# Performance work log

Measured on AMD Instinct MI355X. Metric: run time of the kernel, lower is better.

The kernel has to match this reference:

```python
import jax, jax.numpy as jnp
import numpy as np

B, L, D, H, DFF = 4, 2048, 1024, 16, 4096
DH = D // H  # head dim = 64
EPS = 1e-5


def layernorm(x, g, b):
    mu = jnp.mean(x, axis=-1, keepdims=True)
    var = jnp.mean(jnp.square(x - mu), axis=-1, keepdims=True)
    return (x - mu) * jax.lax.rsqrt(var + EPS) * g + b


def setup_inputs() -> dict:
    key = jax.random.key(0)
    ks = jax.random.split(key, 16)
    s = 0.02
    return {
        "X": jax.random.normal(ks[0], (B, L, D), jnp.float32),
        "WQ": jax.random.normal(ks[1], (D, D), jnp.float32) * s,
        "bQ": jnp.zeros((D,), jnp.float32),
        "WK": jax.random.normal(ks[2], (D, D), jnp.float32) * s,
        "bK": jnp.zeros((D,), jnp.float32),
        "WV": jax.random.normal(ks[3], (D, D), jnp.float32) * s,
        "bV": jnp.zeros((D,), jnp.float32),
        "WO": jax.random.normal(ks[4], (D, D), jnp.float32) * s,
        "bO": jnp.zeros((D,), jnp.float32),
        "W1": jax.random.normal(ks[5], (D, DFF), jnp.float32) * s,
        "b1": jnp.zeros((DFF,), jnp.float32),
        "W2": jax.random.normal(ks[6], (DFF, D), jnp.float32) * s,
        "b2": jnp.zeros((D,), jnp.float32),
        "g1": jnp.ones((D,), jnp.float32),
        "be1": jnp.zeros((D,), jnp.float32),
        "g2": jnp.ones((D,), jnp.float32),
        "be2": jnp.zeros((D,), jnp.float32),
    }


def reference(X, WQ, bQ, WK, bK, WV, bV, WO, bO, W1, b1, W2, b2, g1, be1, g2, be2):
    # --- causal self-attention on LayerNorm1(X) ---
    Xn = layernorm(X, g1, be1)
    def heads(W, b):
        return (Xn @ W + b).reshape(B, L, H, DH).transpose(0, 2, 1, 3)  # [B,H,L,DH]
    Q, K, V = heads(WQ, bQ), heads(WK, bK), heads(WV, bV)
    scale = 1.0 / jnp.sqrt(jnp.float32(DH))
    scores = jnp.einsum('bhld,bhsd->bhls', Q, K) * scale  # [B,H,L,L]
    causal = jnp.tril(jnp.ones((L, L), dtype=bool))
    scores = jnp.where(causal, scores, -jnp.inf)
    attn = jax.nn.softmax(scores, axis=-1)
    AV = jnp.einsum('bhls,bhsd->bhld', attn, V)  # [B,H,L,DH]
    AV = AV.transpose(0, 2, 1, 3).reshape(B, L, H * DH)
    X = X + AV @ WO + bO
    # --- MLP on LayerNorm2(X) ---
    Xn2 = layernorm(X, g2, be2)
    out = X + jax.nn.relu(Xn2 @ W1 + b1) @ W2 + b2
    return out
```

## Files before the change

kernel.cpp:

```cpp
#include <hip/hip_runtime.h>
#include <hip/hip_bf16.h>
#include <stdint.h>

#define B_   4
#define L_   2048
#define D_   1024
#define H_   16
#define DH_  64
#define DFF_ 4096
#define EPS_ 1e-5f

typedef short s16x8 __attribute__((ext_vector_type(8)));
typedef short s16x4 __attribute__((ext_vector_type(4)));
typedef float f32x4 __attribute__((ext_vector_type(4)));

static __device__ __forceinline__ short f2bf(float f) {
    return __builtin_bit_cast(short, __float2bfloat16(f));
}

static __device__ __forceinline__ void gload_lds16(const void* g, void* l) {
    __builtin_amdgcn_global_load_lds(
        (const __attribute__((address_space(1))) uint32_t*)g,
        (__attribute__((address_space(3))) uint32_t*)l, 16, 0, 0);
}

__global__ __launch_bounds__(256) void transpose_kernel(
    const float* __restrict__ in, short* __restrict__ out, int R, int C)
{
    __shared__ float tile[32][33];
    const int bx = blockIdx.x * 32, by = blockIdx.y * 32;
    const int tx = threadIdx.x & 31, ty = threadIdx.x >> 5;
#pragma unroll
    for (int i = 0; i < 32; i += 8)
        tile[ty + i][tx] = in[(size_t)(by + ty + i) * C + bx + tx];
    __syncthreads();
#pragma unroll
    for (int i = 0; i < 32; i += 8)
        out[(size_t)(bx + ty + i) * R + by + tx] = f2bf(tile[tx][ty + i]);
}

__global__ __launch_bounds__(256) void concat3_kernel(
    const float* __restrict__ a, const float* __restrict__ b,
    const float* __restrict__ c, float* __restrict__ o)
{
    const int i = blockIdx.x * 256 + threadIdx.x;
    o[i] = (i < 1024) ? a[i] : (i < 2048 ? b[i - 1024] : c[i - 2048]);
}

__global__ __launch_bounds__(256) void vtrans_kernel(
    const short* __restrict__ V, short* __restrict__ Vt)
{
    __shared__ short t[64][72];
    const int l0 = blockIdx.x * 64;
    const int bh = blockIdx.y;
    const int b = bh >> 4, h = bh & 15;
    const int tid = threadIdx.x;
    const int rr = tid >> 3, cc = tid & 7;
#pragma unroll
    for (int i = 0; i < 2; ++i) {
        const int row = i * 32 + rr;
        *(s16x8*)&t[row][cc * 8] =
            *(const s16x8*)(V + (size_t)(b * L_ + l0 + row) * D_ + h * DH_ + cc * 8);
    }
    __syncthreads();
#pragma unroll
    for (int i = 0; i < 2; ++i) {
        const int d = i * 32 + rr;
        const int lp0 = cc * 8;
        s16x8 o;
#pragma unroll
        for (int j = 0; j < 8; ++j) o[j] = t[lp0 + j][d];
        *(s16x8*)(Vt + ((size_t)bh * DH_ + d) * L_ + l0 + lp0) = o;
    }
}

__global__ __launch_bounds__(256) void ln_kernel(
    const float* __restrict__ x, const float* __restrict__ g,
    const float* __restrict__ bta, short* __restrict__ out)
{
    __shared__ float sm[8];
    const int row = blockIdx.x;
    const int t = threadIdx.x;
    const float4 v = ((const float4*)(x + (size_t)row * D_))[t];
    float s1 = v.x + v.y + v.z + v.w;
    float s2 = v.x * v.x + v.y * v.y + v.z * v.z + v.w * v.w;
#pragma unroll
    for (int off = 1; off < 64; off <<= 1) {
        s1 += __shfl_xor(s1, off);
        s2 += __shfl_xor(s2, off);
    }
    if ((t & 63) == 0) { sm[t >> 6] = s1; sm[4 + (t >> 6)] = s2; }
    __syncthreads();
    s1 = sm[0] + sm[1] + sm[2] + sm[3];
    s2 = sm[4] + sm[5] + sm[6] + sm[7];
    const float mu  = s1 * (1.f / D_);
    const float var = s2 * (1.f / D_) - mu * mu;
    const float rs  = rsqrtf(var + EPS_);
    const float4 gv = ((const float4*)g)[t];
    const float4 bv = ((const float4*)bta)[t];
    s16x4 o;
    o[0] = f2bf((v.x - mu) * rs * gv.x + bv.x);
    o[1] = f2bf((v.y - mu) * rs * gv.y + bv.y);
    o[2] = f2bf((v.z - mu) * rs * gv.z + bv.z);
    o[3] = f2bf((v.w - mu) * rs * gv.w + bv.w);
    *(s16x4*)(out + (size_t)row * D_ + t * 4) = o;
}

template <int MODE>
__global__ __launch_bounds__(512) void gemm_kernel(
    const short* __restrict__ A, const short* __restrict__ Bt,
    const float* __restrict__ bias, const float* __restrict__ res,
    void* __restrict__ out, int M, int N, int K)
{
    __shared__ short As[3][128 * 32];
    __shared__ short Bs[3][256 * 32];
    const int m0 = blockIdx.y * 128;
    const int n0 = blockIdx.x * 256;
    const int tid = threadIdx.x;
    const int w = tid >> 6, l = tid & 63;
    const int wm = w >> 2, wn = w & 3;
    const int lg = l >> 4, li = l & 15;

    const int arow = tid >> 2;
    const int ach = (tid & 3) ^ ((arow >> 1) & 3);
    const short* aSrc = A + (size_t)(m0 + arow) * K + ach * 8;
    const int adst = tid * 8;
    const short* bSrc[2];
    int bdst[2];
#pragma unroll
    for (int i = 0; i < 2; ++i) {
        const int cid = i * 512 + tid;
        const int row = cid >> 2;
        const int ch = (cid & 3) ^ ((row >> 1) & 3);
        bSrc[i] = Bt + (size_t)(n0 + row) * K + ch * 8;
        bdst[i] = cid * 8;
    }

    int aoff[4], boff[4];
#pragma unroll
    for (int m = 0; m < 4; ++m) {
        const int rowA = wm * 64 + m * 16 + li;
        aoff[m] = rowA * 32 + ((lg ^ ((rowA >> 1) & 3)) * 8);
    }
#pragma unroll
    for (int n = 0; n < 4; ++n) {
        const int rowB = wn * 64 + n * 16 + li;
        boff[n] = rowB * 32 + ((lg ^ ((rowB >> 1) & 3)) * 8);
    }

    f32x4 acc[4][4] = {};
    const int nT = K >> 5;

    gload_lds16(aSrc, &As[0][adst]);
#pragma unroll
    for (int i = 0; i < 2; ++i) gload_lds16(bSrc[i], &Bs[0][bdst[i]]);

    int cur = 0, nxt = 1;
    for (int t = 0; t < nT; ++t) {
        if (t + 1 < nT) {
            const int k1 = (t + 1) << 5;
            gload_lds16(aSrc + k1, &As[nxt][adst]);
#pragma unroll
            for (int i = 0; i < 2; ++i) gload_lds16(bSrc[i] + k1, &Bs[nxt][bdst[i]]);
            asm volatile("s_waitcnt vmcnt(3)" ::: "memory");
        } else {
            asm volatile("s_waitcnt vmcnt(0)" ::: "memory");
        }
        __builtin_amdgcn_s_barrier();
        __builtin_amdgcn_sched_barrier(0);

        const short* as = &As[cur][0];
        const short* bs = &Bs[cur][0];
        s16x8 af[4], bf[4];
#pragma unroll
        for (int m = 0; m < 4; ++m) af[m] = *(const s16x8*)&as[aoff[m]];
#pragma unroll
        for (int n = 0; n < 4; ++n) bf[n] = *(const s16x8*)&bs[boff[n]];
#pragma unroll
        for (int m = 0; m < 4; ++m)
#pragma unroll
            for (int n = 0; n < 4; ++n)
                acc[m][n] = __builtin_amdgcn_mfma_f32_16x16x32_bf16(
                    af[m], bf[n], acc[m][n], 0, 0, 0);

        cur = nxt;
        nxt = (nxt == 2) ? 0 : nxt + 1;
    }

#pragma unroll
    for (int m = 0; m < 4; ++m) {
#pragma unroll
        for (int n = 0; n < 4; ++n) {
            const int col = n0 + wn * 64 + n * 16 + li;
            const float bv = bias[col];
#pragma unroll
            for (int r = 0; r < 4; ++r) {
                const int row = m0 + wm * 64 + m * 16 + lg * 4 + r;
                float v = acc[m][n][r] + bv;
                if (MODE == 1) v = v > 0.f ? v : 0.f;
                if (MODE == 2) {
                    float* o = (float*)out;
                    o[(size_t)row * N + col] = v + res[(size_t)row * N + col];
                } else if (MODE == 3) {
                    short* o = (short*)out;
                    o[(size_t)(col >> 10) * (8192ull * 1024) +
                      (size_t)row * 1024 + (col & 1023)] = f2bf(v);
                } else {
                    short* o = (short*)out;
                    o[(size_t)row * N + col] = f2bf(v);
                }
            }
        }
    }
}

__global__ __launch_bounds__(512) void attn_kernel(
    const short* __restrict__ Q, const short* __restrict__ K,
    const short* __restrict__ Vt, short* __restrict__ O)
{
    __shared__ short Kbuf[3][64 * 64];
    __shared__ short Vbuf[3][64 * 64];
    __shared__ short Ps[8][16 * 72];

    const int xx = blockIdx.x;
    const int pr = xx >> 1;
    const int qblk = (xx & 1) ? (15 - pr) : pr;
    const int h = blockIdx.y, b = blockIdx.z;
    const int tid = threadIdx.x;
    const int w = tid >> 6, l = tid & 63;
    const int lg = l >> 4, li = l & 15;
    const size_t headQ = ((size_t)b * L_) * D_ + (size_t)h * DH_;
    const size_t headV = ((size_t)(b * H_ + h) * DH_) * L_;
    const int q0 = qblk * 128;
    const int qw = q0 + w * 16;
    const float scale = 0.125f;

    s16x8 qf[2];
    {
        const short* qr = Q + headQ + (size_t)(qw + li) * D_;
        qf[0] = *(const s16x8*)(qr + lg * 8);
        qf[1] = *(const s16x8*)(qr + 32 + lg * 8);
    }

    const int srow = tid >> 3;
    const int schk = (tid & 7) ^ (srow & 7);
    const short* kSrc = K + headQ + (size_t)srow * D_ + schk * 8;
    const short* vSrc = Vt + headV + (size_t)srow * L_ + schk * 8;

    int koff0[4], koff1[4];
#pragma unroll
    for (int blk = 0; blk < 4; ++blk) {
        const int row = blk * 16 + li;
        const int hh = row & 7;
        koff0[blk] = row * 64 + ((lg ^ hh) * 8);
        koff1[blk] = row * 64 + (((lg + 4) ^ hh) * 8);
    }

    float m_r = -1e30f, l_r = 0.f;
    f32x4 oacc[4] = {};
    short* pw = &Ps[w][0];

    const int nt = 2 * qblk + 2;

    gload_lds16(kSrc, &Kbuf[0][tid * 8]);
    gload_lds16(vSrc, &Vbuf[0][tid * 8]);

    int cur = 0, nxt = 1;
    for (int t = 0; t < nt; ++t) {
        const int kv0 = t * 64;
        if (t + 1 < nt) {
            const int nkv = kv0 + 64;
            gload_lds16(kSrc + (size_t)nkv * D_, &Kbuf[nxt][tid * 8]);
            gload_lds16(vSrc + nkv, &Vbuf[nxt][tid * 8]);
            asm volatile("s_waitcnt vmcnt(2)" ::: "memory");
        } else {
            asm volatile("s_waitcnt vmcnt(0)" ::: "memory");
        }
        __builtin_amdgcn_s_barrier();
        __builtin_amdgcn_sched_barrier(0);

        const short* kb = &Kbuf[cur][0];
        const short* vb = &Vbuf[cur][0];

        f32x4 s[4];
        __builtin_amdgcn_s_setprio(1);
#pragma unroll
        for (int blk = 0; blk < 4; ++blk) {
            const s16x8 kf0 = *(const s16x8*)&kb[koff0[blk]];
            const s16x8 kf1 = *(const s16x8*)&kb[koff1[blk]];
            f32x4 c = {0.f, 0.f, 0.f, 0.f};
            c = __builtin_amdgcn_mfma_f32_16x16x32_bf16(kf0, qf[0], c, 0, 0, 0);
            c = __builtin_amdgcn_mfma_f32_16x16x32_bf16(kf1, qf[1], c, 0, 0, 0);
            s[blk] = c;
        }
        __builtin_amdgcn_s_setprio(0);

        if (kv0 + 63 > qw) {
            const int q = qw + li;
#pragma unroll
            for (int blk = 0; blk < 4; ++blk) {
                const int kvb = kv0 + blk * 16 + lg * 4;
#pragma unroll
                for (int r = 0; r < 4; ++r)
                    if (kvb + r > q) s[blk][r] = -1e30f;
            }
        }

        float mm = fmaxf(fmaxf(s[0][0], s[0][1]), fmaxf(s[0][2], s[0][3]));
#pragma unroll
        for (int blk = 1; blk < 4; ++blk)
            mm = fmaxf(mm, fmaxf(fmaxf(s[blk][0], s[blk][1]),
                                 fmaxf(s[blk][2], s[blk][3])));
        mm = fmaxf(mm, __shfl_xor(mm, 16));
        mm = fmaxf(mm, __shfl_xor(mm, 32));
        const float mxs = mm * scale;

        float p[4][4];
        if (__all(mxs <= m_r + 8.0f)) {
            float sum = 0.f;
#pragma unroll
            for (int blk = 0; blk < 4; ++blk)
#pragma unroll
                for (int r = 0; r < 4; ++r) {
                    p[blk][r] = __expf(fmaf(s[blk][r], scale, -m_r));
                    sum += p[blk][r];
                }
            sum += __shfl_xor(sum, 16);
            sum += __shfl_xor(sum, 32);
            l_r += sum;
        } else {
            const float mn = fmaxf(m_r, mxs);
            const float fac = __expf(m_r - mn);
            m_r = mn;
            float sum = 0.f;
#pragma unroll
            for (int blk = 0; blk < 4; ++blk)
#pragma unroll
                for (int r = 0; r < 4; ++r) {
                    p[blk][r] = __expf(fmaf(s[blk][r], scale, -mn));
                    sum += p[blk][r];
                }
            sum += __shfl_xor(sum, 16);
            sum += __shfl_xor(sum, 32);
            l_r = l_r * fac + sum;
#pragma unroll
            for (int d = 0; d < 4; ++d)
#pragma unroll
                for (int r = 0; r < 4; ++r)
                    oacc[d][r] *= fac;
        }

#pragma unroll
        for (int blk = 0; blk < 4; ++blk) {
            s16x4 pk;
#pragma unroll
            for (int r = 0; r < 4; ++r) pk[r] = f2bf(p[blk][r]);
            *(s16x4*)&pw[li * 72 + blk * 16 + lg * 4] = pk;
        }
        asm volatile("s_waitcnt lgkmcnt(0)" ::: "memory");
        __builtin_amdgcn_sched_barrier(0);
        const s16x8 pa0 = *(const s16x8*)&pw[li * 72 + lg * 8];
        const s16x8 pa1 = *(const s16x8*)&pw[li * 72 + 32 + lg * 8];

        __builtin_amdgcn_s_setprio(1);
#pragma unroll
        for (int dblk = 0; dblk < 4; ++dblk) {
            const s16x8 vf0 = *(const s16x8*)&vb[koff0[dblk]];
            const s16x8 vf1 = *(const s16x8*)&vb[koff1[dblk]];
            oacc[dblk] = __builtin_amdgcn_mfma_f32_16x16x32_bf16(vf0, pa0, oacc[dblk], 0, 0, 0);
            oacc[dblk] = __builtin_amdgcn_mfma_f32_16x16x32_bf16(vf1, pa1, oacc[dblk], 0, 0, 0);
        }
        __builtin_amdgcn_s_setprio(0);

        cur = nxt;
        nxt = (nxt == 2) ? 0 : nxt + 1;
    }

    const float inv = 1.f / l_r;
#pragma unroll
    for (int dblk = 0; dblk < 4; ++dblk) {
        s16x4 ov;
#pragma unroll
        for (int r = 0; r < 4; ++r) ov[r] = f2bf(oacc[dblk][r] * inv);
        *(s16x4*)(O + headQ + (size_t)(qw + li) * D_ + dblk * 16 + lg * 4) = ov;
    }
}

extern "C" void kernel_launch(void* const* d_in, const int* in_sizes, int n_in,
                              void* d_out, int out_size, void* d_ws, size_t ws_size,
                              hipStream_t stream)
{
    const float* X   = (const float*)d_in[0];
    const float* WQ  = (const float*)d_in[1];
    const float* bQ  = (const float*)d_in[2];
    const float* WK  = (const float*)d_in[3];
    const float* bK  = (const float*)d_in[4];
    const float* WV  = (const float*)d_in[5];
    const float* bV  = (const float*)d_in[6];
    const float* WO  = (const float*)d_in[7];
    const float* bO  = (const float*)d_in[8];
    const float* W1  = (const float*)d_in[9];
    const float* b1  = (const float*)d_in[10];
    const float* W2  = (const float*)d_in[11];
    const float* b2  = (const float*)d_in[12];
    const float* g1  = (const float*)d_in[13];
    const float* be1 = (const float*)d_in[14];
    const float* g2  = (const float*)d_in[15];
    const float* be2 = (const float*)d_in[16];
    float* out = (float*)d_out;

    char* ws = (char*)d_ws;
    const size_t MB = 1u << 20;
    short* WQKVt = (short*)(ws + 0 * MB);
    short* WOt = (short*)(ws + 6 * MB);
    short* W1t = (short*)(ws + 8 * MB);
    short* W2t = (short*)(ws + 16 * MB);
    short* Xn  = (short*)(ws + 24 * MB);
    short* Qb  = (short*)(ws + 40 * MB);
    short* Vb  = (short*)(ws + 72 * MB);
    short* Vtb = (short*)(ws + 88 * MB);
    float* bQKV = (float*)(ws + 88 * MB);
    short* AV  = (short*)(ws + 72 * MB);
    short* H1  = (short*)(ws + 40 * MB);

    const dim3 tb(256);

    transpose_kernel<<<dim3(32, 32), tb, 0, stream>>>(WQ, WQKVt, 1024, 1024);
    transpose_kernel<<<dim3(32, 32), tb, 0, stream>>>(WK, WQKVt + 1024 * 1024, 1024, 1024);
    transpose_kernel<<<dim3(32, 32), tb, 0, stream>>>(WV, WQKVt + 2 * 1024 * 1024, 1024, 1024);
    transpose_kernel<<<dim3(32, 32), tb, 0, stream>>>(WO, WOt, 1024, 1024);
    transpose_kernel<<<dim3(128, 32), tb, 0, stream>>>(W1, W1t, 1024, 4096);
    transpose_kernel<<<dim3(32, 128), tb, 0, stream>>>(W2, W2t, 4096, 1024);
    concat3_kernel<<<dim3(12), tb, 0, stream>>>(bQ, bK, bV, bQKV);

    ln_kernel<<<8192, tb, 0, stream>>>(X, g1, be1, Xn);

    gemm_kernel<3><<<dim3(12, 64), dim3(512), 0, stream>>>(
        Xn, WQKVt, bQKV, nullptr, Qb, 8192, 3072, 1024);

    vtrans_kernel<<<dim3(L_ / 64, B_ * H_), tb, 0, stream>>>(Vb, Vtb);

    attn_kernel<<<dim3(L_ / 128, H_, B_), dim3(512), 0, stream>>>(
        Qb, Qb + 8192ull * 1024, Vtb, AV);

    gemm_kernel<2><<<dim3(4, 64), dim3(512), 0, stream>>>(
        AV, WOt, bO, X, out, 8192, 1024, 1024);

    ln_kernel<<<8192, tb, 0, stream>>>(out, g2, be2, Xn);

    gemm_kernel<1><<<dim3(16, 64), dim3(512), 0, stream>>>(
        Xn, W1t, b1, nullptr, H1, 8192, 4096, 1024);
    gemm_kernel<2><<<dim3(4, 64), dim3(512), 0, stream>>>(
        H1, W2t, b2, out, out, 8192, 1024, 4096);
}
```

Before: 424.8 us.

## Replace GEMM with 256-row, K=64 ping-pong pipelined kernel using quarter-phase staging

```diff
diff --git a/kernel.cpp b/kernel.cpp
--- a/kernel.cpp
+++ b/kernel.cpp
@@ -106,96 +106,162 @@
     *(s16x4*)(out + (size_t)row * D_ + t * 4) = o;
 }
 
-template <int MODE>
-__global__ __launch_bounds__(512) void gemm_kernel(
+template <int MODE, int BN, int WM, int WN>
+__global__ __launch_bounds__(512, 2) void gemm8_kernel(
     const short* __restrict__ A, const short* __restrict__ Bt,
     const float* __restrict__ bias, const float* __restrict__ res,
     void* __restrict__ out, int M, int N, int K)
 {
-    __shared__ short As[3][128 * 32];
-    __shared__ short Bs[3][256 * 32];
-    const int m0 = blockIdx.y * 128;
-    const int n0 = blockIdx.x * 256;
+    constexpr int MR = 256 / (16 * WM);
+    constexpr int NR = BN / (16 * WN);
+    constexpr int MH = MR / 2, NH = NR / 2;
+    constexpr int BHALF = BN / 2;
+    constexpr int LB = (BN == 256) ? 2 : 1;
+    constexpr int NHOFF = BHALF * 64;
+
+    __shared__ short As[2][256 * 64];
+    __shared__ short Bs[2][BN * 64];
+
+    const int m0 = blockIdx.y * 256;
+    const int n0 = blockIdx.x * BN;
     const int tid = threadIdx.x;
     const int w = tid >> 6, l = tid & 63;
-    const int wm = w >> 2, wn = w & 3;
+    const int wm = w / WN, wn = w % WN;
     const int lg = l >> 4, li = l & 15;
 
-    const int arow = tid >> 2;
-    const int ach = (tid & 3) ^ ((arow >> 1) & 3);
-    const short* aSrc = A + (size_t)(m0 + arow) * K + ach * 8;
-    const int adst = tid * 8;
-    const short* bSrc[2];
-    int bdst[2];
+    const short* aB[2]; int aD[2];
 #pragma unroll
     for (int i = 0; i < 2; ++i) {
-        const int cid = i * 512 + tid;
-        const int row = cid >> 2;
-        const int ch = (cid & 3) ^ ((row >> 1) & 3);
-        bSrc[i] = Bt + (size_t)(n0 + row) * K + ch * 8;
-        bdst[i] = cid * 8;
-    }
-
-    int aoff[4], boff[4];
-#pragma unroll
-    for (int m = 0; m < 4; ++m) {
-        const int rowA = wm * 64 + m * 16 + li;
-        aoff[m] = rowA * 32 + ((lg ^ ((rowA >> 1) & 3)) * 8);
-    }
-#pragma unroll
-    for (int n = 0; n < 4; ++n) {
-        const int rowB = wn * 64 + n * 16 + li;
-        boff[n] = rowB * 32 + ((lg ^ ((rowB >> 1) & 3)) * 8);
-    }
-
-    f32x4 acc[4][4] = {};
-    const int nT = K >> 5;
-
-    gload_lds16(aSrc, &As[0][adst]);
-#pragma unroll
-    for (int i = 0; i < 2; ++i) gload_lds16(bSrc[i], &Bs[0][bdst[i]]);
-
-    int cur = 0, nxt = 1;
+        const int s = i * 512 + tid;
+        const int row = s >> 3, ch = (s & 7) ^ (row & 7);
+        aB[i] = A + (size_t)(m0 + row) * K + ch * 8;
+        aD[i] = s * 8;
+    }
+    const short* bB[LB]; int bD[LB];
+#pragma unroll
+    for (int i = 0; i < LB; ++i) {
+        const int s = i * 512 + tid;
+        const int row = s >> 3, ch = (s & 7) ^ (row & 7);
+        bB[i] = Bt + (size_t)(n0 + row) * K + ch * 8;
+        bD[i] = s * 8;
+    }
+
+    int aoff[MH][2], boff[NH][2];
+#pragma unroll
+    for (int mm = 0; mm < MH; ++mm)
+#pragma unroll
+        for (int ks = 0; ks < 2; ++ks) {
+            const int r = wm * 16 + mm * (16 * WM) + li;
+            const int c = ks * 4 + lg;
+            aoff[mm][ks] = r * 64 + ((c ^ (r & 7)) * 8);
+        }
+#pragma unroll
+    for (int nn = 0; nn < NH; ++nn)
+#pragma unroll
+        for (int ks = 0; ks < 2; ++ks) {
+            const int r = wn * 16 + nn * (16 * WN) + li;
+            const int c = ks * 4 + lg;
+            boff[nn][ks] = r * 64 + ((c ^ (r & 7)) * 8);
+        }
+
+    f32x4 acc[MR][NR] = {};
+    s16x8 af[MH][2], bf[NH][2];
+    const int nT = K >> 6;
+
+#define STAGE_A(BUF, HALF, KT) do {                                           \
+    _Pragma("unroll")                                                         \
+    for (int i = 0; i < 2; ++i)                                               \
+        gload_lds16(aB[i] + (size_t)(HALF) * 128 * K + (KT) * 64,             \
+                    &As[BUF][(HALF) * 8192 + aD[i]]); } while (0)
+#define STAGE_B(BUF, HALF, KT) do {                                           \
+    _Pragma("unroll")                                                         \
+    for (int i = 0; i < LB; ++i)                                              \
+        gload_lds16(bB[i] + (size_t)(HALF) * BHALF * K + (KT) * 64,           \
+                    &Bs[BUF][(HALF) * NHOFF + bD[i]]); } while (0)
+#define LDA8(MOFF) do {                                                       \
+    _Pragma("unroll")                                                         \
+    for (int mm = 0; mm < MH; ++mm)                                           \
+        _Pragma("unroll")                                                     \
+        for (int ks = 0; ks < 2; ++ks)                                        \
+            af[mm][ks] = *(const s16x8*)&as[(MOFF) + aoff[mm][ks]]; } while (0)
+#define LDB8(NOFF) do {                                                       \
+    _Pragma("unroll")                                                         \
+    for (int nn = 0; nn < NH; ++nn)                                           \
+        _Pragma("unroll")                                                     \
+        for (int ks = 0; ks < 2; ++ks)                                        \
+            bf[nn][ks] = *(const s16x8*)&bs[(NOFF) + boff[nn][ks]]; } while (0)
+#define MMA8(MB, NB) do {                                                     \
+    __builtin_amdgcn_s_setprio(1);                                            \
+    _Pragma("unroll")                                                         \
+    for (int mm = 0; mm < MH; ++mm)                                           \
+        _Pragma("unroll")                                                     \
+        for (int nn = 0; nn < NH; ++nn)                                       \
+            _Pragma("unroll")                                                 \
+            for (int ks = 0; ks < 2; ++ks)                                    \
+                acc[(MB) + mm][(NB) + nn] =                                   \
+                    __builtin_amdgcn_mfma_f32_16x16x32_bf16(                  \
+                        af[mm][ks], bf[nn][ks], acc[(MB) + mm][(NB) + nn],    \
+                        0, 0, 0);                                             \
+    __builtin_amdgcn_s_setprio(0); } while (0)
+#define VMW() do {                                                            \
+    if constexpr (LB == 2) asm volatile("s_waitcnt vmcnt(6)" ::: "memory");   \
+    else                   asm volatile("s_waitcnt vmcnt(5)" ::: "memory");   \
+    } while (0)
+#define PHASE_SYNC do {                                                       \
+    asm volatile("" ::: "memory");                                            \
+    __builtin_amdgcn_s_barrier();                                             \
+    asm volatile("s_waitcnt lgkmcnt(0)" ::: "memory");                        \
+    __builtin_amdgcn_sched_barrier(0); } while (0)
+#define PHASE_END do {                                                        \
+    asm volatile("" ::: "memory");                                            \
+    __builtin_amdgcn_s_barrier(); } while (0)
+
+    STAGE_A(0, 0, 0); STAGE_B(0, 1, 0); STAGE_A(0, 1, 0); STAGE_B(0, 0, 0);
+    STAGE_A(1, 0, 1); STAGE_B(1, 1, 1); STAGE_A(1, 1, 1);
+    VMW();
+    __builtin_amdgcn_s_barrier();
+
     for (int t = 0; t < nT; ++t) {
-        if (t + 1 < nT) {
-            const int k1 = (t + 1) << 5;
-            gload_lds16(aSrc + k1, &As[nxt][adst]);
-#pragma unroll
-            for (int i = 0; i < 2; ++i) gload_lds16(bSrc[i] + k1, &Bs[nxt][bdst[i]]);
-            asm volatile("s_waitcnt vmcnt(3)" ::: "memory");
-        } else {
-            asm volatile("s_waitcnt vmcnt(0)" ::: "memory");
-        }
-        __builtin_amdgcn_s_barrier();
-        __builtin_amdgcn_sched_barrier(0);
-
-        const short* as = &As[cur][0];
-        const short* bs = &Bs[cur][0];
-        s16x8 af[4], bf[4];
-#pragma unroll
-        for (int m = 0; m < 4; ++m) af[m] = *(const s16x8*)&as[aoff[m]];
-#pragma unroll
-        for (int n = 0; n < 4; ++n) bf[n] = *(const s16x8*)&bs[boff[n]];
-#pragma unroll
-        for (int m = 0; m < 4; ++m)
-#pragma unroll
-            for (int n = 0; n < 4; ++n)
-                acc[m][n] = __builtin_amdgcn_mfma_f32_16x16x32_bf16(
-                    af[m], bf[n], acc[m][n], 0, 0, 0);
-
-        cur = nxt;
-        nxt = (nxt == 2) ? 0 : nxt + 1;
-    }
-
-#pragma unroll
-    for (int m = 0; m < 4; ++m) {
-#pragma unroll
-        for (int n = 0; n < 4; ++n) {
-            const int col = n0 + wn * 64 + n * 16 + li;
+        const int buf = t & 1, nbuf = buf ^ 1;
+        const short* as = &As[buf][0];
+        const short* bs = &Bs[buf][0];
+        const int tn = (t + 1 < nT) ? t + 1 : nT - 1;
+        const int tc = (t + 2 < nT) ? t + 2 : nT - 1;
+        LDA8(0); LDB8(0);
+        STAGE_B(nbuf, 0, tn);
+        PHASE_SYNC; MMA8(0, 0); PHASE_END;
+        LDB8(NHOFF);
+        STAGE_A(buf, 0, tc);
+        PHASE_SYNC; MMA8(0, NH); PHASE_END;
+        LDA8(8192);
+        STAGE_B(buf, 1, tc);
+        PHASE_SYNC; MMA8(MH, NH); PHASE_END;
+        LDB8(0);
+        STAGE_A(buf, 1, tc);
+        PHASE_SYNC; MMA8(MH, 0);
+        VMW();
+        PHASE_END;
+    }
+
+#undef STAGE_A
+#undef STAGE_B
+#undef LDA8
+#undef LDB8
+#undef MMA8
+#undef VMW
+#undef PHASE_SYNC
+#undef PHASE_END
+
+#pragma unroll
+    for (int m = 0; m < MR; ++m) {
+        const int row0 = m0 + wm * 16 + m * (16 * WM) + lg * 4;
+#pragma unroll
+        for (int n = 0; n < NR; ++n) {
+            const int col = n0 + wn * 16 + n * (16 * WN) + li;
             const float bv = bias[col];
 #pragma unroll
             for (int r = 0; r < 4; ++r) {
-                const int row = m0 + wm * 64 + m * 16 + lg * 4 + r;
+                const int row = row0 + r;
                 float v = acc[m][n][r] + bv;
                 if (MODE == 1) v = v > 0.f ? v : 0.f;
                 if (MODE == 2) {
@@ -435,7 +501,7 @@
 
     ln_kernel<<<8192, tb, 0, stream>>>(X, g1, be1, Xn);
 
-    gemm_kernel<3><<<dim3(12, 64), dim3(512), 0, stream>>>(
+    gemm8_kernel<3, 256, 2, 4><<<dim3(12, 32), dim3(512), 0, stream>>>(
         Xn, WQKVt, bQKV, nullptr, Qb, 8192, 3072, 1024);
 
     vtrans_kernel<<<dim3(L_ / 64, B_ * H_), tb, 0, stream>>>(Vb, Vtb);
@@ -443,13 +509,13 @@
     attn_kernel<<<dim3(L_ / 128, H_, B_), dim3(512), 0, stream>>>(
         Qb, Qb + 8192ull * 1024, Vtb, AV);
 
-    gemm_kernel<2><<<dim3(4, 64), dim3(512), 0, stream>>>(
+    gemm8_kernel<2, 128, 4, 2><<<dim3(8, 32), dim3(512), 0, stream>>>(
         AV, WOt, bO, X, out, 8192, 1024, 1024);
 
     ln_kernel<<<8192, tb, 0, stream>>>(out, g2, be2, Xn);
 
-    gemm_kernel<1><<<dim3(16, 64), dim3(512), 0, stream>>>(
+    gemm8_kernel<1, 256, 2, 4><<<dim3(16, 32), dim3(512), 0, stream>>>(
         Xn, W1t, b1, nullptr, H1, 8192, 4096, 1024);
-    gemm_kernel<2><<<dim3(4, 64), dim3(512), 0, stream>>>(
+    gemm8_kernel<2, 128, 4, 2><<<dim3(8, 32), dim3(512), 0, stream>>>(
         H1, W2t, b2, out, out, 8192, 1024, 4096);
 }
```

Result: slower. 488.1 us (+14.9%).
